# Kernel tuning notes

Hardware: AMD Instinct MI355X
Metric: run time of the kernel (lower is better)

Reference implementation:

```python
import jax, jax.numpy as jnp
import numpy as np
import math

D_MODEL, D_STATE, D_CONV, EXPAND = 1024, 64, 4, 2
D_INNER = EXPAND * D_MODEL
DT_RANK = math.ceil(D_MODEL / 8)
B_SZ, L_SEQ = 2, 4096


def setup_inputs() -> dict:
    key = jax.random.key(0)
    ks = jax.random.split(key, 8)
    hidden_states = jax.random.normal(ks[0], (B_SZ, L_SEQ, D_MODEL), jnp.float32)
    in_proj_w = jax.random.normal(ks[1], (2 * D_INNER, D_MODEL), jnp.float32) * (D_MODEL ** -0.5)
    conv_w = jax.random.normal(ks[2], (D_INNER, 1, D_CONV), jnp.float32) * (D_CONV ** -0.5)
    conv_b = jnp.zeros((D_INNER,), jnp.float32)
    x_proj_w = jax.random.normal(ks[3], (DT_RANK + 2 * D_STATE, D_INNER), jnp.float32) * (D_INNER ** -0.5)
    dt_init_std = DT_RANK ** -0.5
    dt_proj_w = jax.random.uniform(ks[4], (D_INNER, DT_RANK), jnp.float32, -dt_init_std, dt_init_std)
    # inverse-softplus init of dt bias, as in the torch module
    dt = jnp.exp(jax.random.uniform(ks[5], (D_INNER,), jnp.float32) * (math.log(0.1) - math.log(0.001)) + math.log(0.001))
    dt = jnp.clip(dt, 1e-4, None)
    dt_proj_b = dt + jnp.log(-jnp.expm1(-dt))
    A_log = jnp.log(jnp.broadcast_to(jnp.arange(1, D_STATE + 1, dtype=jnp.float32), (D_INNER, D_STATE)))
    D = jnp.ones((D_INNER,), jnp.float32)
    out_proj_w = jax.random.normal(ks[6], (D_MODEL, D_INNER), jnp.float32) * (D_INNER ** -0.5)
    return dict(hidden_states=hidden_states, in_proj_w=in_proj_w, conv_w=conv_w, conv_b=conv_b,
                x_proj_w=x_proj_w, dt_proj_w=dt_proj_w, dt_proj_b=dt_proj_b,
                A_log=A_log, D=D, out_proj_w=out_proj_w)


def _mamba_fwd(hidden_states, in_proj_w, conv_w, conv_b, x_proj_w, dt_proj_w, dt_proj_b, A_log, D, out_proj_w):
    b, l, _ = hidden_states.shape
    d_inner, d_state = A_log.shape
    dt_rank = dt_proj_w.shape[1]
    xz = hidden_states @ in_proj_w.T                      # (b, l, 2*d_inner)
    x, z = xz[..., :d_inner], xz[..., d_inner:]
    # causal depthwise conv over time
    xc = jax.lax.conv_general_dilated(
        x.transpose(0, 2, 1), conv_w, window_strides=(1,),
        padding=[(conv_w.shape[-1] - 1, 0)],
        dimension_numbers=('NCH', 'OIH', 'NCH'),
        feature_group_count=d_inner) + conv_b[None, :, None]
    x = jax.nn.silu(xc).transpose(0, 2, 1)                # (b, l, d_inner)
    x_dbl = x @ x_proj_w.T                                # (b, l, dt_rank + 2*d_state)
    dt_low = x_dbl[..., :dt_rank]
    Bmat = x_dbl[..., dt_rank:dt_rank + d_state]          # (b, l, n)
    Cmat = x_dbl[..., dt_rank + d_state:]                 # (b, l, n)
    dt = jax.nn.softplus(dt_low @ dt_proj_w.T + dt_proj_b)  # (b, l, d_inner)
    A = -jnp.exp(A_log)                                   # (d_inner, n)

    def step(h, inp):
        x_t, dt_t, B_t, C_t = inp                         # (b,d), (b,d), (b,n), (b,n)
        dA = jnp.exp(dt_t[..., None] * A)                 # (b, d, n)
        h = h * dA + (dt_t * x_t)[..., None] * B_t[:, None, :]
        y = jnp.einsum('bdn,bn->bd', h, C_t)
        return h, y

    xs = (x.transpose(1, 0, 2), dt.transpose(1, 0, 2), Bmat.transpose(1, 0, 2), Cmat.transpose(1, 0, 2))
    h0 = jnp.zeros((b, d_inner, d_state), x.dtype)
    _, ys = jax.lax.scan(step, h0, xs)                    # (l, b, d_inner)
    y = ys.transpose(1, 0, 2) + D * x
    y = y * jax.nn.silu(z)
    return y @ out_proj_w.T                               # (b, l, d_model)


def reference(hidden_states, in_proj_w, conv_w, conv_b, x_proj_w, dt_proj_w, dt_proj_b, A_log, D, out_proj_w):
    return _mamba_fwd(hidden_states, in_proj_w, conv_w, conv_b, x_proj_w, dt_proj_w, dt_proj_b, A_log, D, out_proj_w)
```

## Files before the change

### kernel.cpp

```cpp
#include <hip/hip_runtime.h>
#include <math.h>

#define B_SZ 2
#define L_SEQ 4096
#define D_MODEL 1024
#define D_INNER 2048
#define D_STATE 64
#define DT_RANK 128
#define BL (B_SZ * L_SEQ)

#define AS1 __attribute__((address_space(1)))
#define AS3 __attribute__((address_space(3)))

typedef __attribute__((ext_vector_type(8))) short bf16x8_t;
typedef __attribute__((ext_vector_type(4))) float f32x4_t;

__device__ __forceinline__ unsigned short f2bf(float f) {
    unsigned int u = __float_as_uint(f);
    u = (u + 0x7FFFu + ((u >> 16) & 1u)) >> 16;
    return (unsigned short)u;
}
__device__ __forceinline__ float bf2f(unsigned short h) {
    return __uint_as_float(((unsigned int)h) << 16);
}

__global__ __launch_bounds__(256) void cvt_f32_bf16(
    const float* __restrict__ in, unsigned short* __restrict__ out, int n4)
{
    int i = blockIdx.x * 256 + threadIdx.x;
    if (i >= n4) return;
    float4 v = ((const float4*)in)[i];
    ushort4 o;
    o.x = f2bf(v.x); o.y = f2bf(v.y); o.z = f2bf(v.z); o.w = f2bf(v.w);
    ((ushort4*)out)[i] = o;
}

__global__ __launch_bounds__(256) void cvt_dtpart(
    const float* __restrict__ xdbl, unsigned short* __restrict__ out)
{
    int i = blockIdx.x * 256 + threadIdx.x;
    int m = i >> 5, c = i & 31;
    float4 v = *(const float4*)(xdbl + (size_t)m * 256 + c * 4);
    ushort4 o;
    o.x = f2bf(v.x); o.y = f2bf(v.y); o.z = f2bf(v.z); o.w = f2bf(v.w);
    ((ushort4*)(out))[(size_t)m * 32 + c] = o;
}

__global__ __launch_bounds__(256) void gemm_bf16(
    const unsigned short* __restrict__ A, int lda,
    const unsigned short* __restrict__ B, int ldb,
    float* __restrict__ C, int ldc, int K,
    const float* __restrict__ bias, int act)
{
    __shared__ unsigned short As[128 * 32];
    __shared__ unsigned short Bs[128 * 32];

    const int tid = threadIdx.x;
    const int w = tid >> 6, lane = tid & 63;
    const int bm = blockIdx.y * 128, bn = blockIdx.x * 128;
    const int wm = (w & 1) * 64, wn = (w >> 1) * 64;

    f32x4_t acc[4][4];
#pragma unroll
    for (int i = 0; i < 4; ++i)
#pragma unroll
        for (int j = 0; j < 4; ++j) acc[i][j] = (f32x4_t){0.f, 0.f, 0.f, 0.f};

    const int srow = lane >> 2;
    const int scol = (lane & 3) * 8;
    const unsigned short* Ag0 = A + (size_t)(bm + w * 16 + srow) * lda + scol;
    const unsigned short* Ag1 = A + (size_t)(bm + 64 + w * 16 + srow) * lda + scol;
    const unsigned short* Bg0 = B + (size_t)(bn + w * 16 + srow) * ldb + scol;
    const unsigned short* Bg1 = B + (size_t)(bn + 64 + w * 16 + srow) * ldb + scol;
    unsigned short* la0 = &As[(w * 16) * 32];
    unsigned short* la1 = &As[(64 + w * 16) * 32];
    unsigned short* lb0 = &Bs[(w * 16) * 32];
    unsigned short* lb1 = &Bs[(64 + w * 16) * 32];

    const int fr = lane & 15;
    const int fk = (lane >> 4) * 8;

    for (int k0 = 0; k0 < K; k0 += 32) {
        __syncthreads();
        __builtin_amdgcn_global_load_lds((const AS1 void*)(Ag0 + k0), (AS3 void*)la0, 16, 0, 0);
        __builtin_amdgcn_global_load_lds((const AS1 void*)(Ag1 + k0), (AS3 void*)la1, 16, 0, 0);
        __builtin_amdgcn_global_load_lds((const AS1 void*)(Bg0 + k0), (AS3 void*)lb0, 16, 0, 0);
        __builtin_amdgcn_global_load_lds((const AS1 void*)(Bg1 + k0), (AS3 void*)lb1, 16, 0, 0);
        __syncthreads();

        bf16x8_t af[4], bfr[4];
#pragma unroll
        for (int i = 0; i < 4; ++i)
            af[i] = *(const bf16x8_t*)&As[(wm + i * 16 + fr) * 32 + fk];
#pragma unroll
        for (int j = 0; j < 4; ++j)
            bfr[j] = *(const bf16x8_t*)&Bs[(wn + j * 16 + fr) * 32 + fk];
#pragma unroll
        for (int i = 0; i < 4; ++i)
#pragma unroll
            for (int j = 0; j < 4; ++j)
                acc[i][j] = __builtin_amdgcn_mfma_f32_16x16x32_bf16(
                    af[i], bfr[j], acc[i][j], 0, 0, 0);
    }

    const int erow = (lane >> 4) * 4;
    const int ecol = lane & 15;
#pragma unroll
    for (int i = 0; i < 4; ++i) {
        int gr0 = bm + wm + i * 16 + erow;
#pragma unroll
        for (int j = 0; j < 4; ++j) {
            int gc = bn + wn + j * 16 + ecol;
#pragma unroll
            for (int r = 0; r < 4; ++r) {
                float v = acc[i][j][r];
                if (act == 1) {
                    float t = v + bias[gr0 + r];
                    v = (t > 20.f) ? t : log1pf(__expf(t));
                } else if (act == 2) {
                    v = v / (1.f + __expf(-v));
                }
                C[(size_t)(gr0 + r) * ldc + gc] = v;
            }
        }
    }
}

__global__ __launch_bounds__(256) void conv_silu_kernel(
    const float* __restrict__ xT,
    const float* __restrict__ w,
    const float* __restrict__ bias,
    unsigned short* __restrict__ xcT16)
{
    int gid = blockIdx.x * blockDim.x + threadIdx.x;
    int d = gid >> 11;
    int c4 = gid & 2047;
    int m0 = c4 * 4;
    int l0 = m0 & (L_SEQ - 1);

    const float* row = xT + (size_t)d * BL;
    float4 v = *(const float4*)(row + m0);
    float4 p;
    if (l0 == 0) { p.x = p.y = p.z = p.w = 0.f; }
    else         { p = *(const float4*)(row + m0 - 4); }

    float4 wv = ((const float4*)w)[d];
    float bb = bias[d];
    float e[4];
    e[0] = bb + wv.x * p.y + wv.y * p.z + wv.z * p.w + wv.w * v.x;
    e[1] = bb + wv.x * p.z + wv.y * p.w + wv.z * v.x + wv.w * v.y;
    e[2] = bb + wv.x * p.w + wv.y * v.x + wv.z * v.y + wv.w * v.z;
    e[3] = bb + wv.x * v.x + wv.y * v.y + wv.z * v.z + wv.w * v.w;
    ushort4 o;
    o.x = f2bf(e[0] / (1.f + __expf(-e[0])));
    o.y = f2bf(e[1] / (1.f + __expf(-e[1])));
    o.z = f2bf(e[2] / (1.f + __expf(-e[2])));
    o.w = f2bf(e[3] / (1.f + __expf(-e[3])));
    ((ushort4*)(xcT16 + (size_t)d * BL))[c4] = o;
}

__global__ __launch_bounds__(256) void transpose_f32_bf16(
    const float* __restrict__ in, int ldin,
    unsigned short* __restrict__ out, int ldout)
{
    __shared__ float tl[32][33];
    int r0 = blockIdx.y * 32, c0 = blockIdx.x * 32;
    int tx = threadIdx.x & 31, ty = threadIdx.x >> 5;
#pragma unroll
    for (int k = 0; k < 4; ++k)
        tl[ty + 8 * k][tx] = in[(size_t)(r0 + ty + 8 * k) * ldin + c0 + tx];
    __syncthreads();
#pragma unroll
    for (int k = 0; k < 4; ++k)
        out[(size_t)(c0 + ty + 8 * k) * ldout + r0 + tx] = f2bf(tl[tx][ty + 8 * k]);
}

__global__ __launch_bounds__(256) void transpose_bf16(
    const unsigned short* __restrict__ in, int ldin,
    unsigned short* __restrict__ out, int ldout)
{
    __shared__ unsigned short tl[32][33];
    int r0 = blockIdx.y * 32, c0 = blockIdx.x * 32;
    int tx = threadIdx.x & 31, ty = threadIdx.x >> 5;
#pragma unroll
    for (int k = 0; k < 4; ++k)
        tl[ty + 8 * k][tx] = in[(size_t)(r0 + ty + 8 * k) * ldin + c0 + tx];
    __syncthreads();
#pragma unroll
    for (int k = 0; k < 4; ++k)
        out[(size_t)(c0 + ty + 8 * k) * ldout + r0 + tx] = tl[tx][ty + 8 * k];
}

#define SCHUNK 512

#define GROUP16(BC, CC, BN, CN, GG)                                          \
{                                                                            \
    const float* bn_ = bc + 16 * 256;                                        \
    _Pragma("unroll")                                                        \
    for (int t = 0; t < 16; ++t) {                                           \
        BN[t] = bn_[t * 256];                                                \
        CN[t] = bn_[t * 256 + D_STATE];                                      \
    }                                                                        \
    float4 dta = *(const float4*)&sdt[(GG)];                                 \
    float4 dtb = *(const float4*)&sdt[(GG) + 4];                             \
    float4 dtc = *(const float4*)&sdt[(GG) + 8];                             \
    float4 dtd = *(const float4*)&sdt[(GG) + 12];                            \
    uint4 xr0 = *(const uint4*)&sx[(GG)];                                    \
    uint4 xr1 = *(const uint4*)&sx[(GG) + 8];                                \
    float dt16[16] = {dta.x, dta.y, dta.z, dta.w, dtb.x, dtb.y, dtb.z, dtb.w,\
                      dtc.x, dtc.y, dtc.z, dtc.w, dtd.x, dtd.y, dtd.z, dtd.w};\
    float xf[16];                                                            \
    xf[0]  = __uint_as_float(xr0.x << 16); xf[1]  = __uint_as_float(xr0.x & 0xffff0000u); \
    xf[2]  = __uint_as_float(xr0.y << 16); xf[3]  = __uint_as_float(xr0.y & 0xffff0000u); \
    xf[4]  = __uint_as_float(xr0.z << 16); xf[5]  = __uint_as_float(xr0.z & 0xffff0000u); \
    xf[6]  = __uint_as_float(xr0.w << 16); xf[7]  = __uint_as_float(xr0.w & 0xffff0000u); \
    xf[8]  = __uint_as_float(xr1.x << 16); xf[9]  = __uint_as_float(xr1.x & 0xffff0000u); \
    xf[10] = __uint_as_float(xr1.y << 16); xf[11] = __uint_as_float(xr1.y & 0xffff0000u); \
    xf[12] = __uint_as_float(xr1.z << 16); xf[13] = __uint_as_float(xr1.z & 0xffff0000u); \
    xf[14] = __uint_as_float(xr1.w << 16); xf[15] = __uint_as_float(xr1.w & 0xffff0000u); \
    float pr[16];                                                            \
    _Pragma("unroll")                                                        \
    for (int t = 0; t < 16; ++t) {                                           \
        float a = __builtin_amdgcn_exp2f(dt16[t] * An2);                     \
        h = fmaf(h, a, (dt16[t] * xf[t]) * BC[t]);                           \
        pr[t] = h * CC[t];                                                   \
    }                                                                        \
    _Pragma("unroll")                                                        \
    for (int t = 0; t < 8; ++t) {                   \
        float send = (lane & 32) ? pr[t] : pr[t + 8];                        \
        float recv = __shfl_xor(send, 32);                                   \
        pr[t] = ((lane & 32) ? pr[t + 8] : pr[t]) + recv;                    \
    }                                                                        \
    _Pragma("unroll")                                                        \
    for (int t = 0; t < 4; ++t) {                    \
        float send = (lane & 16) ? pr[t] : pr[t + 4];                        \
        float recv = __shfl_xor(send, 16);                                   \
        pr[t] = ((lane & 16) ? pr[t + 4] : pr[t]) + recv;                    \
    }                                                                        \
    _Pragma("unroll")                                                        \
    for (int t = 0; t < 2; ++t) {                     \
        float send = (lane & 8) ? pr[t] : pr[t + 2];                         \
        float recv = __shfl_xor(send, 8);                                    \
        pr[t] = ((lane & 8) ? pr[t + 2] : pr[t]) + recv;                     \
    }                                                                        \
    {                                                 \
        float send = (lane & 4) ? pr[0] : pr[1];                             \
        float recv = __shfl_xor(send, 4);                                    \
        pr[0] = ((lane & 4) ? pr[1] : pr[0]) + recv;                         \
    }                                                                        \
    pr[0] += __shfl_xor(pr[0], 2);          \
    pr[0] += __shfl_xor(pr[0], 1);                                           \
    if ((lane & 3) == 0) {               \
        int t0 = (GG) + myt16;                                               \
        float xv = bf2f(sx[t0]);                                             \
        float zv = sz[t0];                                                   \
        zrow[cbase + t0] = fmaf(Dd, xv, pr[0]) * zv;                         \
    }                                                                        \
    bc += 16 * 256;                                                          \
}

__global__ __launch_bounds__(256, 4) void scan_seq_kernel(
    const float* __restrict__ dtT,
    const unsigned short* __restrict__ xcT16,
    const float* __restrict__ xdbl,
    float* __restrict__ zyT,
    const float* __restrict__ A_log,
    const float* __restrict__ Dp)
{
    __shared__ __align__(16) float s_dt[4][SCHUNK];
    __shared__ __align__(16) unsigned short s_x[4][SCHUNK];
    __shared__ __align__(16) float s_z[4][SCHUNK];

    const int tid  = threadIdx.x;
    const int wid  = tid >> 6;
    const int lane = tid & 63;
    const int bi   = blockIdx.x;
    const int b    = bi & 1;
    const int d    = (bi >> 1) * 4 + wid;

    const size_t rowbase = (size_t)d * BL + (size_t)b * L_SEQ;
    const float An2 = -__expf(A_log[d * D_STATE + lane]) * 1.44269504f;
    const float Dd  = Dp[d];

    float* sdt = s_dt[wid];
    unsigned short* sx = s_x[wid];
    float* sz = s_z[wid];
    const float* dtrow = dtT + rowbase;
    const unsigned short* xrow = xcT16 + rowbase;
    float* zrow = zyT + rowbase;
    const int myt16 = (lane >> 2) & 15;

    float4 pA = ((const float4*)dtrow)[lane];
    float4 pB = ((const float4*)dtrow)[lane + 64];
    uint4  pX = ((const uint4*)xrow)[lane];
    float4 pZ0 = ((const float4*)zrow)[lane];
    float4 pZ1 = ((const float4*)zrow)[lane + 64];

    const float* bc = xdbl + ((size_t)b * L_SEQ) * 256 + DT_RANK + lane;
    float Bv0[16], Cv0[16], Bv1[16], Cv1[16];
#pragma unroll
    for (int t = 0; t < 16; ++t) { Bv0[t] = bc[t * 256]; Cv0[t] = bc[t * 256 + D_STATE]; }

    float h = 0.f;

    for (int c = 0; c < L_SEQ / SCHUNK; ++c) {
        ((float4*)sdt)[lane]      = pA;
        ((float4*)sdt)[lane + 64] = pB;
        ((uint4*)sx)[lane]        = pX;
        ((float4*)sz)[lane]       = pZ0;
        ((float4*)sz)[lane + 64]  = pZ1;
        if (c < L_SEQ / SCHUNK - 1) {
            pA  = ((const float4*)(dtrow + (c + 1) * SCHUNK))[lane];
            pB  = ((const float4*)(dtrow + (c + 1) * SCHUNK))[lane + 64];
            pX  = ((const uint4*)(xrow + (c + 1) * SCHUNK))[lane];
            pZ0 = ((const float4*)(zrow + (c + 1) * SCHUNK))[lane];
            pZ1 = ((const float4*)(zrow + (c + 1) * SCHUNK))[lane + 64];
        }
        const int cbase = c * SCHUNK;

        for (int g = 0; g < SCHUNK; g += 32) {
            GROUP16(Bv0, Cv0, Bv1, Cv1, g);
            GROUP16(Bv1, Cv1, Bv0, Cv0, g + 16);
        }
    }
}

extern "C" void kernel_launch(void* const* d_in, const int* in_sizes, int n_in,
                              void* d_out, int out_size, void* d_ws, size_t ws_size,
                              hipStream_t stream)
{
    const float* hs        = (const float*)d_in[0];
    const float* in_proj_w = (const float*)d_in[1];
    const float* conv_w    = (const float*)d_in[2];
    const float* conv_b    = (const float*)d_in[3];
    const float* x_proj_w  = (const float*)d_in[4];
    const float* dt_proj_w = (const float*)d_in[5];
    const float* dt_proj_b = (const float*)d_in[6];
    const float* A_log     = (const float*)d_in[7];
    const float* Dp        = (const float*)d_in[8];
    const float* out_proj_w= (const float*)d_in[9];
    float* out = (float*)d_out;

    char* ws = (char*)d_ws;
    const size_t MiB = 1024 * 1024;
    float*          xT    = (float*)(ws);
    unsigned short* xc16  = (unsigned short*)(ws);
    float*          dtT   = (float*)(ws);
    float*          zT    = (float*)(ws + 64 * MiB);
    unsigned short* W1_16 = (unsigned short*)(ws + 128 * MiB);
    unsigned short* hs16  = (unsigned short*)(ws + 136 * MiB);
    unsigned short* xcT16 = (unsigned short*)(ws + 128 * MiB);
    unsigned short* y16   = (unsigned short*)(ws + 128 * MiB);
    float*          xdbl  = (float*)(ws + 160 * MiB);
    unsigned short* xdbl16= (unsigned short*)(ws + 169 * MiB);
    unsigned short* Wx16  = (unsigned short*)(ws + 171 * MiB);
    unsigned short* Wdt16 = (unsigned short*)(ws + 172 * MiB);
    unsigned short* Wo16  = (unsigned short*)(ws + 173 * MiB);

    dim3 blk(256);

    cvt_f32_bf16<<<8192, blk, 0, stream>>>(hs, hs16, 2097152);
    cvt_f32_bf16<<<4096, blk, 0, stream>>>(in_proj_w, W1_16, 1048576);
    cvt_f32_bf16<<<512, blk, 0, stream>>>(x_proj_w, Wx16, 131072);
    cvt_f32_bf16<<<256, blk, 0, stream>>>(dt_proj_w, Wdt16, 65536);
    cvt_f32_bf16<<<2048, blk, 0, stream>>>(out_proj_w, Wo16, 524288);

    gemm_bf16<<<dim3(64, 16), blk, 0, stream>>>(
        W1_16, D_MODEL, hs16, D_MODEL, xT, BL, D_MODEL, nullptr, 0);

    gemm_bf16<<<dim3(64, 16), blk, 0, stream>>>(
        W1_16 + (size_t)D_INNER * D_MODEL, D_MODEL, hs16, D_MODEL,
        zT, BL, D_MODEL, nullptr, 2);

    conv_silu_kernel<<<(D_INNER * (BL / 4)) / 256, blk, 0, stream>>>(
        xT, conv_w, conv_b, xcT16);

    transpose_bf16<<<dim3(BL / 32, D_INNER / 32), blk, 0, stream>>>(
        xcT16, BL, xc16, D_INNER);

    gemm_bf16<<<dim3(2, 64), blk, 0, stream>>>(
        xc16, D_INNER, Wx16, D_INNER, xdbl, 256, D_INNER, nullptr, 0);

    cvt_dtpart<<<1024, blk, 0, stream>>>(xdbl, xdbl16);

    gemm_bf16<<<dim3(64, 16), blk, 0, stream>>>(
        Wdt16, DT_RANK, xdbl16, DT_RANK, dtT, BL, DT_RANK, dt_proj_b, 1);

    scan_seq_kernel<<<(B_SZ * D_INNER) / 4, blk, 0, stream>>>(
        dtT, xcT16, xdbl, zT, A_log, Dp);

    transpose_f32_bf16<<<dim3(BL / 32, D_INNER / 32), blk, 0, stream>>>(
        zT, BL, y16, D_INNER);

    gemm_bf16<<<dim3(8, 64), blk, 0, stream>>>(
        y16, D_INNER, Wo16, D_INNER, out, D_MODEL, D_INNER, nullptr, 0);
}
```

Before: 913.8 us.

## Precompute dt*x per chunk, buffer y in LDS, write gated output per chunk

The scan kernel now computes dt*x once per chunk into a new shared buffer, so the inner recurrence no longer unpacks bf16 x or multiplies by dt for each state lane. Scalar per-timestep global stores of the gated output are replaced by writes to an LDS y buffer, followed by one coalesced float4 multiply-by-z and store at the end of each chunk. The z prefetch is dropped in favour of a direct load at the top of each chunk, and B/C addressing uses a 32-bit unsigned offset. This adds LDS usage, which may reduce occupancy, and the z load is no longer overlapped with the previous chunk.

```diff
diff --git a/kernel.cpp b/kernel.cpp
--- a/kernel.cpp
+++ b/kernel.cpp
@@ -195,34 +195,29 @@
 
 #define GROUP16(BC, CC, BN, CN, GG)                                          \
 {                                                                            \
-    const float* bn_ = bc + 16 * 256;                                        \
     _Pragma("unroll")                                                        \
-    for (int t = 0; t < 16; ++t) {                                           \
-        BN[t] = bn_[t * 256];                                                \
-        CN[t] = bn_[t * 256 + D_STATE];                                      \
-    }                                                                        \
+    for (int t = 0; t < 16; ++t) {          \
+        BN[t] = xb[bo + t * 256u];                                           \
+        CN[t] = xb[bo + t * 256u + 64u];                                     \
+    }                                                                        \
+    bo += 16u * 256u;                                                        \
     float4 dta = *(const float4*)&sdt[(GG)];                                 \
     float4 dtb = *(const float4*)&sdt[(GG) + 4];                             \
     float4 dtc = *(const float4*)&sdt[(GG) + 8];                             \
     float4 dtd = *(const float4*)&sdt[(GG) + 12];                            \
-    uint4 xr0 = *(const uint4*)&sx[(GG)];                                    \
-    uint4 xr1 = *(const uint4*)&sx[(GG) + 8];                                \
+    float4 dxa = *(const float4*)&sdtx[(GG)];                                \
+    float4 dxb = *(const float4*)&sdtx[(GG) + 4];                            \
+    float4 dxc = *(const float4*)&sdtx[(GG) + 8];                            \
+    float4 dxd = *(const float4*)&sdtx[(GG) + 12];                           \
     float dt16[16] = {dta.x, dta.y, dta.z, dta.w, dtb.x, dtb.y, dtb.z, dtb.w,\
                       dtc.x, dtc.y, dtc.z, dtc.w, dtd.x, dtd.y, dtd.z, dtd.w};\
-    float xf[16];                                                            \
-    xf[0]  = __uint_as_float(xr0.x << 16); xf[1]  = __uint_as_float(xr0.x & 0xffff0000u); \
-    xf[2]  = __uint_as_float(xr0.y << 16); xf[3]  = __uint_as_float(xr0.y & 0xffff0000u); \
-    xf[4]  = __uint_as_float(xr0.z << 16); xf[5]  = __uint_as_float(xr0.z & 0xffff0000u); \
-    xf[6]  = __uint_as_float(xr0.w << 16); xf[7]  = __uint_as_float(xr0.w & 0xffff0000u); \
-    xf[8]  = __uint_as_float(xr1.x << 16); xf[9]  = __uint_as_float(xr1.x & 0xffff0000u); \
-    xf[10] = __uint_as_float(xr1.y << 16); xf[11] = __uint_as_float(xr1.y & 0xffff0000u); \
-    xf[12] = __uint_as_float(xr1.z << 16); xf[13] = __uint_as_float(xr1.z & 0xffff0000u); \
-    xf[14] = __uint_as_float(xr1.w << 16); xf[15] = __uint_as_float(xr1.w & 0xffff0000u); \
+    float dx16[16] = {dxa.x, dxa.y, dxa.z, dxa.w, dxb.x, dxb.y, dxb.z, dxb.w,\
+                      dxc.x, dxc.y, dxc.z, dxc.w, dxd.x, dxd.y, dxd.z, dxd.w};\
     float pr[16];                                                            \
     _Pragma("unroll")                                                        \
     for (int t = 0; t < 16; ++t) {                                           \
         float a = __builtin_amdgcn_exp2f(dt16[t] * An2);                     \
-        h = fmaf(h, a, (dt16[t] * xf[t]) * BC[t]);                           \
+        h = fmaf(h, a, dx16[t] * BC[t]);                                     \
         pr[t] = h * CC[t];                                                   \
     }                                                                        \
     _Pragma("unroll")                                                        \
@@ -253,10 +248,8 @@
     if ((lane & 3) == 0) {               \
         int t0 = (GG) + myt16;                                               \
         float xv = bf2f(sx[t0]);                                             \
-        float zv = sz[t0];                                                   \
-        zrow[cbase + t0] = fmaf(Dd, xv, pr[0]) * zv;                         \
-    }                                                                        \
-    bc += 16 * 256;                                                          \
+        sy[t0] = fmaf(Dd, xv, pr[0]);                                        \
+    }                                                                        \
 }
 
 __global__ __launch_bounds__(256, 4) void scan_seq_kernel(
@@ -268,8 +261,9 @@
     const float* __restrict__ Dp)
 {
     __shared__ __align__(16) float s_dt[4][SCHUNK];
+    __shared__ __align__(16) float s_dtx[4][SCHUNK];
     __shared__ __align__(16) unsigned short s_x[4][SCHUNK];
-    __shared__ __align__(16) float s_z[4][SCHUNK];
+    __shared__ __align__(16) float s_y[4][SCHUNK];
 
     const int tid  = threadIdx.x;
     const int wid  = tid >> 6;
@@ -283,8 +277,9 @@
     const float Dd  = Dp[d];
 
     float* sdt = s_dt[wid];
+    float* sdtx = s_dtx[wid];
     unsigned short* sx = s_x[wid];
-    float* sz = s_z[wid];
+    float* sy = s_y[wid];
     const float* dtrow = dtT + rowbase;
     const unsigned short* xrow = xcT16 + rowbase;
     float* zrow = zyT + rowbase;
@@ -292,29 +287,39 @@
 
     float4 pA = ((const float4*)dtrow)[lane];
     float4 pB = ((const float4*)dtrow)[lane + 64];
-    uint4  pX = ((const uint4*)xrow)[lane];
-    float4 pZ0 = ((const float4*)zrow)[lane];
-    float4 pZ1 = ((const float4*)zrow)[lane + 64];
-
-    const float* bc = xdbl + ((size_t)b * L_SEQ) * 256 + DT_RANK + lane;
+    ushort4 pX0 = ((const ushort4*)xrow)[lane];
+    ushort4 pX1 = ((const ushort4*)xrow)[lane + 64];
+
+    const float* __restrict__ xb = xdbl;
+    unsigned bo = (unsigned)(b * L_SEQ) * 256u + DT_RANK + (unsigned)lane;
     float Bv0[16], Cv0[16], Bv1[16], Cv1[16];
 #pragma unroll
-    for (int t = 0; t < 16; ++t) { Bv0[t] = bc[t * 256]; Cv0[t] = bc[t * 256 + D_STATE]; }
+    for (int t = 0; t < 16; ++t) { Bv0[t] = xb[bo + t * 256u]; Cv0[t] = xb[bo + t * 256u + 64u]; }
+    bo += 16u * 256u;
 
     float h = 0.f;
 
     for (int c = 0; c < L_SEQ / SCHUNK; ++c) {
+        float4 z0 = ((const float4*)(zrow + c * SCHUNK))[lane];
+        float4 z1 = ((const float4*)(zrow + c * SCHUNK))[lane + 64];
+
         ((float4*)sdt)[lane]      = pA;
         ((float4*)sdt)[lane + 64] = pB;
-        ((uint4*)sx)[lane]        = pX;
-        ((float4*)sz)[lane]       = pZ0;
-        ((float4*)sz)[lane + 64]  = pZ1;
+        ((ushort4*)sx)[lane]      = pX0;
+        ((ushort4*)sx)[lane + 64] = pX1;
+        float4 dxA, dxB;
+        dxA.x = pA.x * bf2f(pX0.x); dxA.y = pA.y * bf2f(pX0.y);
+        dxA.z = pA.z * bf2f(pX0.z); dxA.w = pA.w * bf2f(pX0.w);
+        dxB.x = pB.x * bf2f(pX1.x); dxB.y = pB.y * bf2f(pX1.y);
+        dxB.z = pB.z * bf2f(pX1.z); dxB.w = pB.w * bf2f(pX1.w);
+        ((float4*)sdtx)[lane]      = dxA;
+        ((float4*)sdtx)[lane + 64] = dxB;
+
         if (c < L_SEQ / SCHUNK - 1) {
             pA  = ((const float4*)(dtrow + (c + 1) * SCHUNK))[lane];
             pB  = ((const float4*)(dtrow + (c + 1) * SCHUNK))[lane + 64];
-            pX  = ((const uint4*)(xrow + (c + 1) * SCHUNK))[lane];
-            pZ0 = ((const float4*)(zrow + (c + 1) * SCHUNK))[lane];
-            pZ1 = ((const float4*)(zrow + (c + 1) * SCHUNK))[lane + 64];
+            pX0 = ((const ushort4*)(xrow + (c + 1) * SCHUNK))[lane];
+            pX1 = ((const ushort4*)(xrow + (c + 1) * SCHUNK))[lane + 64];
         }
         const int cbase = c * SCHUNK;
 
@@ -322,6 +327,13 @@
             GROUP16(Bv0, Cv0, Bv1, Cv1, g);
             GROUP16(Bv1, Cv1, Bv0, Cv0, g + 16);
         }
+
+        float4 y0 = ((const float4*)sy)[lane];
+        float4 y1 = ((const float4*)sy)[lane + 64];
+        y0.x *= z0.x; y0.y *= z0.y; y0.z *= z0.z; y0.w *= z0.w;
+        y1.x *= z1.x; y1.y *= z1.y; y1.z *= z1.z; y1.w *= z1.w;
+        ((float4*)(zrow + cbase))[lane]      = y0;
+        ((float4*)(zrow + cbase))[lane + 64] = y1;
     }
 }
 
```

After: 924.2 us. About the same (+1.1%).

## Use permlane swaps for scan reductions and 16-wave lockstep scan blocks

Applied to the files above, without the earlier changes.

Replaces the first two cross-lane reduction stages in the selective scan with permlane32/permlane16 swap builtins, where available, instead of shfl_xor plus selects. Each scan block grows from 4 to 16 waves (1024 threads), one channel per wave, and a barrier after every 32 timesteps keeps the waves in lockstep so they share B/C loads through cache. It also pads the dt shared buffer pitch. The risks are barrier stalls, lower scheduling flexibility with 1024-thread blocks, and the runtime probe used to pick the swap direction.

```diff
diff --git a/kernel.cpp b/kernel.cpp
--- a/kernel.cpp
+++ b/kernel.cpp
@@ -14,6 +14,7 @@
 
 typedef __attribute__((ext_vector_type(8))) short bf16x8_t;
 typedef __attribute__((ext_vector_type(4))) float f32x4_t;
+typedef __attribute__((ext_vector_type(2))) unsigned int u32x2_t;
 
 __device__ __forceinline__ unsigned short f2bf(float f) {
     unsigned int u = __float_as_uint(f);
@@ -192,6 +193,24 @@
 }
 
 #define SCHUNK 512
+#define SDT_PITCH 544
+
+#if __has_builtin(__builtin_amdgcn_permlane32_swap)
+#define HAVE_PL32 1
+__device__ __forceinline__ float pl32_fold(float x, float y) {
+    u32x2_t r = __builtin_amdgcn_permlane32_swap(
+        __float_as_uint(x), __float_as_uint(y), false, false);
+    return __uint_as_float(r.x) + __uint_as_float(r.y);
+}
+#endif
+#if __has_builtin(__builtin_amdgcn_permlane16_swap)
+#define HAVE_PL16 1
+__device__ __forceinline__ float pl16_fold(float x, float y) {
+    u32x2_t r = __builtin_amdgcn_permlane16_swap(
+        __float_as_uint(x), __float_as_uint(y), false, false);
+    return __uint_as_float(r.x) + __uint_as_float(r.y);
+}
+#endif
 
 #define GROUP16(BC, CC, BN, CN, GG)                                          \
 {                                                                            \
@@ -225,18 +244,8 @@
         h = fmaf(h, a, (dt16[t] * xf[t]) * BC[t]);                           \
         pr[t] = h * CC[t];                                                   \
     }                                                                        \
-    _Pragma("unroll")                                                        \
-    for (int t = 0; t < 8; ++t) {                   \
-        float send = (lane & 32) ? pr[t] : pr[t + 8];                        \
-        float recv = __shfl_xor(send, 32);                                   \
-        pr[t] = ((lane & 32) ? pr[t + 8] : pr[t]) + recv;                    \
-    }                                                                        \
-    _Pragma("unroll")                                                        \
-    for (int t = 0; t < 4; ++t) {                    \
-        float send = (lane & 16) ? pr[t] : pr[t + 4];                        \
-        float recv = __shfl_xor(send, 16);                                   \
-        pr[t] = ((lane & 16) ? pr[t + 4] : pr[t]) + recv;                    \
-    }                                                                        \
+    FOLD_STAGE1;                                                             \
+    FOLD_STAGE2;                                                             \
     _Pragma("unroll")                                                        \
     for (int t = 0; t < 2; ++t) {                     \
         float send = (lane & 8) ? pr[t] : pr[t + 2];                         \
@@ -259,7 +268,45 @@
     bc += 16 * 256;                                                          \
 }
 
-__global__ __launch_bounds__(256, 4) void scan_seq_kernel(
+#ifdef HAVE_PL32
+#define FOLD_STAGE1                                                          \
+    if (dir32) {                                                             \
+        _Pragma("unroll")                                                    \
+        for (int t = 0; t < 8; ++t) pr[t] = pl32_fold(pr[t + 8], pr[t]);     \
+    } else {                                                                 \
+        _Pragma("unroll")                                                    \
+        for (int t = 0; t < 8; ++t) pr[t] = pl32_fold(pr[t], pr[t + 8]);     \
+    }
+#else
+#define FOLD_STAGE1                                                          \
+    _Pragma("unroll")                                                        \
+    for (int t = 0; t < 8; ++t) {                                            \
+        float send = (lane & 32) ? pr[t] : pr[t + 8];                        \
+        float recv = __shfl_xor(send, 32);                                   \
+        pr[t] = ((lane & 32) ? pr[t + 8] : pr[t]) + recv;                    \
+    }
+#endif
+
+#ifdef HAVE_PL16
+#define FOLD_STAGE2                                                          \
+    if (dir16) {                                                             \
+        _Pragma("unroll")                                                    \
+        for (int t = 0; t < 4; ++t) pr[t] = pl16_fold(pr[t + 4], pr[t]);     \
+    } else {                                                                 \
+        _Pragma("unroll")                                                    \
+        for (int t = 0; t < 4; ++t) pr[t] = pl16_fold(pr[t], pr[t + 4]);     \
+    }
+#else
+#define FOLD_STAGE2                                                          \
+    _Pragma("unroll")                                                        \
+    for (int t = 0; t < 4; ++t) {                                            \
+        float send = (lane & 16) ? pr[t] : pr[t + 4];                        \
+        float recv = __shfl_xor(send, 16);                                   \
+        pr[t] = ((lane & 16) ? pr[t + 4] : pr[t]) + recv;                    \
+    }
+#endif
+
+__global__ __launch_bounds__(1024) void scan_seq_kernel(
     const float* __restrict__ dtT,
     const unsigned short* __restrict__ xcT16,
     const float* __restrict__ xdbl,
@@ -267,20 +314,37 @@
     const float* __restrict__ A_log,
     const float* __restrict__ Dp)
 {
-    __shared__ __align__(16) float s_dt[4][SCHUNK];
-    __shared__ __align__(16) unsigned short s_x[4][SCHUNK];
-    __shared__ __align__(16) float s_z[4][SCHUNK];
+    __shared__ __align__(16) float s_dt[16][SDT_PITCH];
+    __shared__ __align__(16) unsigned short s_x[16][SCHUNK];
+    __shared__ __align__(16) float s_z[16][SCHUNK];
 
     const int tid  = threadIdx.x;
     const int wid  = tid >> 6;
     const int lane = tid & 63;
     const int bi   = blockIdx.x;
     const int b    = bi & 1;
-    const int d    = (bi >> 1) * 4 + wid;
+    const int d    = (bi >> 1) * 16 + wid;
 
     const size_t rowbase = (size_t)d * BL + (size_t)b * L_SEQ;
     const float An2 = -__expf(A_log[d * D_STATE + lane]) * 1.44269504f;
     const float Dd  = Dp[d];
+
+#ifdef HAVE_PL32
+    bool dir32;
+    {
+        u32x2_t r = __builtin_amdgcn_permlane32_swap((unsigned)lane,
+                        (unsigned)lane + 1000u, false, false);
+        dir32 = (__builtin_amdgcn_readfirstlane(r.x) == 1032u);
+    }
+#endif
+#ifdef HAVE_PL16
+    bool dir16;
+    {
+        u32x2_t r = __builtin_amdgcn_permlane16_swap((unsigned)lane,
+                        (unsigned)lane + 1000u, false, false);
+        dir16 = (__builtin_amdgcn_readfirstlane(r.x) == 1016u);
+    }
+#endif
 
     float* sdt = s_dt[wid];
     unsigned short* sx = s_x[wid];
@@ -321,6 +385,7 @@
         for (int g = 0; g < SCHUNK; g += 32) {
             GROUP16(Bv0, Cv0, Bv1, Cv1, g);
             GROUP16(Bv1, Cv1, Bv0, Cv0, g + 16);
+            __builtin_amdgcn_s_barrier();
         }
     }
 }
@@ -386,7 +451,7 @@
     gemm_bf16<<<dim3(64, 16), blk, 0, stream>>>(
         Wdt16, DT_RANK, xdbl16, DT_RANK, dtT, BL, DT_RANK, dt_proj_b, 1);
 
-    scan_seq_kernel<<<(B_SZ * D_INNER) / 4, blk, 0, stream>>>(
+    scan_seq_kernel<<<256, dim3(1024), 0, stream>>>(
         dtT, xcT16, xdbl, zT, A_log, Dp);
 
     transpose_f32_bf16<<<dim3(BL / 32, D_INNER / 32), blk, 0, stream>>>(
```

After: 981.4 us. 7.4% more time.
